# Kernel optimization log

Hardware: AMD Instinct MI355X
Metric: run time of the kernel (lower is better)

Reference implementation:

```python
import jax, jax.numpy as jnp
import numpy as np
from jax import lax

B, C, H, W = 4, 64, 96, 320
RC = C // 4                     # reduced channels = 16
D = 48                          # max_disp = len(norm_disp_range)
NORM_DISP = jnp.arange(D, dtype=jnp.float32) / 160.0
EPS = 1e-5


def conv2d(x, w, b=None, pad=0, groups=1):
    y = lax.conv_general_dilated(x, w, (1, 1), ((pad, pad), (pad, pad)),
                                 dimension_numbers=('NCHW', 'OIHW', 'NCHW'),
                                 feature_group_count=groups)
    if b is not None:
        y = y + b[None, :, None, None]
    return y


def group_norm(x, g, b, groups=8):
    n, c, h, w = x.shape
    xg = x.reshape(n, groups, c // groups, h, w)
    mu = xg.mean(axis=(2, 3, 4), keepdims=True)
    var = xg.var(axis=(2, 3, 4), keepdims=True)
    xn = ((xg - mu) * lax.rsqrt(var + EPS)).reshape(n, c, h, w)
    return xn * g[None, :, None, None] + b[None, :, None, None]


elu = jax.nn.elu


def setup_inputs() -> dict:
    key = jax.random.key(0)
    ks = iter(jax.random.split(key, 32))

    def rn(shape, scale=0.05):
        return jax.random.normal(next(ks), shape, dtype=jnp.float32) * scale

    inp = {
        'left_feat': jax.random.normal(next(ks), (B, C, H, W), jnp.float32),
        'right_feat': jax.random.normal(next(ks), (B, C, H, W), jnp.float32),
        'directs': jnp.ones((B,), jnp.float32),
        # q_conv / k_conv: 1x1 conv (no bias) + GroupNorm(8) params
        'qw': rn((RC, C, 1, 1)), 'q_g': jnp.ones((RC,)), 'q_b': jnp.zeros((RC,)),
        'kw': rn((RC, C, 1, 1)), 'k_g': jnp.ones((RC,)), 'k_b': jnp.zeros((RC,)),
        # global_attn: avgpool -> 1x1 (rc->rc/2) -> ELU -> 1x1 (rc/2->rc)
        'ga_w1': rn((RC // 2, RC, 1, 1)), 'ga_b1': jnp.zeros((RC // 2,)),
        'ga_w2': rn((RC, RC // 2, 1, 1)), 'ga_b2': jnp.zeros((RC,)),
        # local_attn: 3x3 conv + GN(8) + ELU
        'la_w': rn((RC, RC, 3, 3)), 'la_b': jnp.zeros((RC,)),
        'la_g': jnp.ones((RC,)), 'la_bb': jnp.zeros((RC,)),
        # attn_fusion: 1x1 (2rc->rc) -> ELU -> 1x1 (rc->D)
        'af_w1': rn((RC, 2 * RC, 1, 1)), 'af_b1': jnp.zeros((RC,)),
        'af_w2': rn((D, RC, 1, 1)), 'af_b2': jnp.zeros((D,)),
        # refine_cost: depthwise 3x3 (groups=D) -> ELU -> 1x1
        'rdw_w': rn((D, 1, 3, 3)), 'rdw_b': jnp.zeros((D,)),
        'rpw_w': rn((D, D, 1, 1)), 'rpw_b': jnp.zeros((D,)),
        # fusion: reflection-pad 3x3 conv (C+D -> C) + SELayer(C, 16)
        'fu_w': rn((C, C + D, 3, 3)), 'fu_b': jnp.zeros((C,)),
        'se_w1': rn((C // 16, C)), 'se_w2': rn((C, C // 16)),
    }
    return inp


def reference(left_feat, right_feat, directs, qw, q_g, q_b, kw, k_g, k_b,
              ga_w1, ga_b1, ga_w2, ga_b2, la_w, la_b, la_g, la_bb,
              af_w1, af_b1, af_w2, af_b2, rdw_w, rdw_b, rpw_w, rpw_b,
              fu_w, fu_b, se_w1, se_w2):
    q = elu(group_norm(conv2d(left_feat, qw), q_g, q_b))      # [B,RC,H,W]
    k = elu(group_norm(conv2d(right_feat, kw), k_g, k_b))     # [B,RC,H,W]

    gp = q.mean(axis=(2, 3), keepdims=True)                   # AdaptiveAvgPool2d(1)
    gfeat = conv2d(elu(conv2d(gp, ga_w1, ga_b1)), ga_w2, ga_b2)
    gfeat = jnp.broadcast_to(gfeat, q.shape)
    lfeat = elu(group_norm(conv2d(q, la_w, la_b, pad=1), la_g, la_bb))
    comb = jnp.concatenate([gfeat, lfeat], axis=1)            # [B,2RC,H,W]
    attn = conv2d(elu(conv2d(comb, af_w1, af_b1)), af_w2, af_b2)  # [B,D,H,W]

    # Warped cost volume. grid_sample shifts only the x-coordinate by
    # disp*2*directs (normalized, align_corners=True), i.e. a constant
    # horizontal shift of disp*directs*(W-1) pixels with border clamping.
    # Channel-mean commutes with horizontal bilinear sampling, so warp
    # the channel-mean map directly (identical math, D x less work).
    km = k.mean(axis=1)                                       # [B,H,W]
    shift = NORM_DISP[None, :] * directs[:, None] * (W - 1)   # [B,D]
    pos = jnp.arange(W, dtype=jnp.float32)[None, None, :] + shift[:, :, None]  # [B,D,W]
    x0 = jnp.floor(pos)
    f = pos - x0                                              # bilinear frac
    i0 = jnp.clip(x0, 0, W - 1).astype(jnp.int32)
    i1 = jnp.clip(x0 + 1, 0, W - 1).astype(jnp.int32)

    def gather(idx):  # km[b,h,idx[b,d,w]] -> [B,D,H,W]
        return jnp.take_along_axis(
            km[:, None, :, :],
            jnp.broadcast_to(idx[:, :, None, :], (B, D, H, W)), axis=3)

    fw = f[:, :, None, :]
    warped = gather(i0) * (1.0 - fw) + gather(i1) * fw        # [B,D,H,W]
    vol = warped * jax.nn.sigmoid(attn)                       # sigmoid-weighted volume

    cost = conv2d(elu(conv2d(vol, rdw_w, rdw_b, pad=1, groups=D)), rpw_w, rpw_b)
    norm_cost = jax.nn.softmax(cost, axis=1)

    # fusion: ReflectionPad2d(1) + 3x3 conv, SE layer, ELU
    cat = jnp.concatenate([left_feat, norm_cost], axis=1)     # [B,C+D,H,W]
    cat_p = jnp.pad(cat, ((0, 0), (0, 0), (1, 1), (1, 1)), mode='reflect')
    fused = conv2d(cat_p, fu_w, fu_b)                         # [B,C,H,W]
    y = fused.mean(axis=(2, 3))                               # [B,C]
    y = jax.nn.sigmoid(jax.nn.relu(y @ se_w1.T) @ se_w2.T)
    x = elu(fused * y[:, :, None, None])
    return (x, norm_cost)
```

## Files before the change

kernel.cpp:

```cpp
#include <hip/hip_runtime.h>
#include <math.h>

static constexpr int B_  = 4;
static constexpr int C_  = 64;
static constexpr int H_  = 96;
static constexpr int W_  = 320;
static constexpr int HW  = H_ * W_;
static constexpr int RCH = 16;
static constexpr int D_  = 48;
static constexpr int NG  = 8;
static constexpr int CPG = RCH / NG;
static constexpr float EPS_ = 1e-5f;
static constexpr int APX = 322;

typedef __attribute__((ext_vector_type(8))) short short8;
typedef __attribute__((ext_vector_type(4))) float f32x4;
typedef __attribute__((ext_vector_type(4))) unsigned int u32x4;

__device__ __forceinline__ float elu1(float x) { return x > 0.f ? x : __expf(x) - 1.f; }
__device__ __forceinline__ float sigm(float x) { return 1.f / (1.f + __expf(-x)); }
__device__ __forceinline__ unsigned bf16rne(float f) {
    unsigned u = __builtin_bit_cast(unsigned, f);
    u += 0x7fffu + ((u >> 16) & 1u);
    return u >> 16;
}
__device__ __forceinline__ void gload16(const void* g, void* l) {
    __builtin_amdgcn_global_load_lds((const __attribute__((address_space(1))) unsigned int*)g,
                                     (__attribute__((address_space(3))) unsigned int*)l, 16, 0, 0);
}

__global__ __launch_bounds__(256) void k_wrepack(
    const float* __restrict__ qw, const float* __restrict__ kw, const float* __restrict__ law,
    float* __restrict__ qwp, float* __restrict__ kwp, float* __restrict__ lawp)
{
    int t = threadIdx.x;
    for (int i = t; i < RCH * C_; i += 256) {
        int c = i >> 4, r = i & 15;
        qwp[i] = qw[r * C_ + c];
        kwp[i] = kw[r * C_ + c];
    }
    for (int i = t; i < RCH * RCH * 9; i += 256) {
        int co = i & 15, rest = i >> 4;
        int ci = rest / 9, tap = rest % 9;
        lawp[i] = law[(co * RCH + ci) * 9 + tap];
    }
}

__global__ __launch_bounds__(256) void k_conv_qk(
    const float* __restrict__ left, const float* __restrict__ right,
    const float* __restrict__ qwp, const float* __restrict__ kwp,
    float* __restrict__ qraw, float* __restrict__ kraw)
{
    int idx = blockIdx.x * 256 + threadIdx.x;
    int half = idx / (B_ * HW / 2);
    int r0 = idx - half * (B_ * HW / 2);
    int b = r0 / (HW / 2), p2 = r0 - b * (HW / 2);
    int p = p2 * 2;
    const float* src = (half ? right : left) + (size_t)b * C_ * HW + p;
    const float* wp  = half ? kwp : qwp;
    float* dst = (half ? kraw : qraw) + (size_t)b * RCH * HW + p;
    float2 acc[RCH];
#pragma unroll
    for (int r = 0; r < RCH; r++) acc[r] = make_float2(0.f, 0.f);
#pragma unroll
    for (int c = 0; c < C_; c++) {
        float2 v = *reinterpret_cast<const float2*>(src + (size_t)c * HW);
        const float* wrow = wp + c * RCH;
#pragma unroll
        for (int r = 0; r < RCH; r++) {
            acc[r].x += v.x * wrow[r];
            acc[r].y += v.y * wrow[r];
        }
    }
#pragma unroll
    for (int r = 0; r < RCH; r++)
        *reinterpret_cast<float2*>(dst + (size_t)r * HW) = acc[r];
}

__global__ __launch_bounds__(256) void k_gn_stats2(const float* __restrict__ qsrc,
    const float* __restrict__ ksrc, float* __restrict__ stats)
{
    int z = blockIdx.x;
    const float* src = (z < 32) ? qsrc : ksrc;
    int zz = (z < 32) ? z : z - 32;
    int b = zz / NG, g = zz % NG;
    const float4* base = (const float4*)(src + ((size_t)b * RCH + g * CPG) * HW);
    float s = 0.f, ss = 0.f;
    for (int i = threadIdx.x; i < CPG * HW / 4; i += 256) {
        float4 v = base[i];
        s  += v.x + v.y + v.z + v.w;
        ss += v.x * v.x + v.y * v.y + v.z * v.z + v.w * v.w;
    }
    __shared__ float rs[256], rq[256];
    rs[threadIdx.x] = s; rq[threadIdx.x] = ss; __syncthreads();
    for (int off = 128; off > 0; off >>= 1) {
        if (threadIdx.x < off) { rs[threadIdx.x] += rs[threadIdx.x + off]; rq[threadIdx.x] += rq[threadIdx.x + off]; }
        __syncthreads();
    }
    if (threadIdx.x == 0) {
        float inv = 1.f / (float)(CPG * HW);
        float m = rs[0] * inv;
        float var = rq[0] * inv - m * m;
        stats[z * 2 + 0] = m;
        stats[z * 2 + 1] = rsqrtf(var + EPS_);
    }
}

__global__ __launch_bounds__(256) void k_gn_stats(const float* __restrict__ src, float* __restrict__ stats)
{
    int b = blockIdx.x / NG, g = blockIdx.x % NG;
    const float4* base = (const float4*)(src + ((size_t)b * RCH + g * CPG) * HW);
    float s = 0.f, ss = 0.f;
    for (int i = threadIdx.x; i < CPG * HW / 4; i += 256) {
        float4 v = base[i];
        s  += v.x + v.y + v.z + v.w;
        ss += v.x * v.x + v.y * v.y + v.z * v.z + v.w * v.w;
    }
    __shared__ float rs[256], rq[256];
    rs[threadIdx.x] = s; rq[threadIdx.x] = ss; __syncthreads();
    for (int off = 128; off > 0; off >>= 1) {
        if (threadIdx.x < off) { rs[threadIdx.x] += rs[threadIdx.x + off]; rq[threadIdx.x] += rq[threadIdx.x + off]; }
        __syncthreads();
    }
    if (threadIdx.x == 0) {
        float inv = 1.f / (float)(CPG * HW);
        float m = rs[0] * inv;
        float var = rq[0] * inv - m * m;
        stats[blockIdx.x * 2 + 0] = m;
        stats[blockIdx.x * 2 + 1] = rsqrtf(var + EPS_);
    }
}

__global__ __launch_bounds__(256) void k_gn_apply(float* __restrict__ x, const float* __restrict__ stats,
    const float* __restrict__ gam, const float* __restrict__ bet)
{
    int idx4 = blockIdx.x * 256 + threadIdx.x;
    int b = idx4 / (RCH * HW / 4);
    int rc = (idx4 / (HW / 4)) % RCH;
    int g = rc >> 1;
    float m = stats[(b * NG + g) * 2], is = stats[(b * NG + g) * 2 + 1];
    float ga = gam[rc] * is, be = bet[rc] - m * is * gam[rc];
    float4 v = ((const float4*)x)[idx4];
    v.x = elu1(v.x * ga + be); v.y = elu1(v.y * ga + be);
    v.z = elu1(v.z * ga + be); v.w = elu1(v.w * ga + be);
    ((float4*)x)[idx4] = v;
}

__global__ __launch_bounds__(256) void k_km(const float* __restrict__ kraw, const float* __restrict__ stats,
    const float* __restrict__ gam, const float* __restrict__ bet, float* __restrict__ km)
{
    int idx = blockIdx.x * 256 + threadIdx.x;
    int b = idx / HW, p = idx - b * HW;
    float s = 0.f;
#pragma unroll
    for (int rc = 0; rc < RCH; rc++) {
        int g = rc >> 1;
        float m = stats[(b * NG + g) * 2], is = stats[(b * NG + g) * 2 + 1];
        float v = (kraw[((size_t)b * RCH + rc) * HW + p] - m) * is * gam[rc] + bet[rc];
        s += elu1(v);
    }
    km[idx] = s * (1.f / (float)RCH);
}

__global__ __launch_bounds__(256) void k_rowmean(const float* __restrict__ src, float* __restrict__ out)
{
    const float4* base = (const float4*)(src + (size_t)blockIdx.x * HW);
    float s = 0.f;
    for (int p = threadIdx.x; p < HW / 4; p += 256) {
        float4 v = base[p];
        s += v.x + v.y + v.z + v.w;
    }
    __shared__ float red[256];
    red[threadIdx.x] = s; __syncthreads();
    for (int off = 128; off > 0; off >>= 1) {
        if (threadIdx.x < off) red[threadIdx.x] += red[threadIdx.x + off];
        __syncthreads();
    }
    if (threadIdx.x == 0) out[blockIdx.x] = red[0] * (1.f / (float)HW);
}

__global__ __launch_bounds__(64) void k_gfeat(const float* __restrict__ gp,
    const float* __restrict__ gaw1, const float* __restrict__ gab1,
    const float* __restrict__ gaw2, const float* __restrict__ gab2,
    const float* __restrict__ afw1, const float* __restrict__ afb1,
    float* __restrict__ gbias)
{
    __shared__ float g1[B_ * 8], gf[B_ * RCH];
    int t = threadIdx.x;
    if (t < B_ * 8) {
        int b = t >> 3, o = t & 7;
        float a = gab1[o];
        for (int i = 0; i < RCH; i++) a += gaw1[o * RCH + i] * gp[b * RCH + i];
        g1[b * 8 + o] = elu1(a);
    }
    __syncthreads();
    {
        int b = t >> 4, o = t & 15;
        float a = gab2[o];
        for (int i = 0; i < 8; i++) a += gaw2[o * 8 + i] * g1[b * 8 + i];
        gf[t] = a;
    }
    __syncthreads();
    {
        int b = t >> 4, o = t & 15;
        float a = afb1[o];
        for (int i = 0; i < RCH; i++) a += afw1[o * 2 * RCH + i] * gf[b * RCH + i];
        gbias[t] = a;
    }
}

__global__ __launch_bounds__(256) void k_conv_la(const float* __restrict__ q,
    const float* __restrict__ lawp, const float* __restrict__ lab, float* __restrict__ lraw)
{
    int idx = blockIdx.x * 256 + threadIdx.x;
    int b = idx / HW, p = idx - b * HW;
    int h = p / W_, w = p - h * W_;
    float acc[RCH];
#pragma unroll
    for (int co = 0; co < RCH; co++) acc[co] = lab[co];
#pragma unroll
    for (int ci = 0; ci < RCH; ci++) {
        const float* qb = q + ((size_t)b * RCH + ci) * HW;
#pragma unroll
        for (int kh = 0; kh < 3; kh++) {
            int hh = h + kh - 1;
            if (hh < 0 || hh >= H_) continue;
            float a0 = (w - 1 >= 0) ? qb[hh * W_ + w - 1] : 0.f;
            float a1 = qb[hh * W_ + w];
            float a2 = (w + 1 < W_) ? qb[hh * W_ + w + 1] : 0.f;
            const float* wp0 = lawp + (ci * 9 + kh * 3) * RCH;
#pragma unroll
            for (int co = 0; co < RCH; co++)
                acc[co] += a0 * wp0[co] + a1 * wp0[RCH + co] + a2 * wp0[2 * RCH + co];
        }
    }
#pragma unroll
    for (int co = 0; co < RCH; co++) lraw[((size_t)b * RCH + co) * HW + p] = acc[co];
}

__global__ __launch_bounds__(320) void k_vol(const float* __restrict__ lraw,
    const float* __restrict__ stats, const float* __restrict__ lg, const float* __restrict__ lb,
    const float* __restrict__ gbias, const float* __restrict__ afw1,
    const float* __restrict__ afw2, const float* __restrict__ afb2,
    const float* __restrict__ km, const float* __restrict__ directs, float* __restrict__ vol)
{
    __shared__ float w1[RCH * 2 * RCH];
    __shared__ float w2[D_ * RCH];
    __shared__ float b2[D_];
    __shared__ float kms[W_];
    int blk = blockIdx.x;
    int b = blk / H_, h = blk - b * H_;
    int t = threadIdx.x;
    for (int i = t; i < RCH * 2 * RCH; i += 320) w1[i] = afw1[i];
    for (int i = t; i < D_ * RCH; i += 320) w2[i] = afw2[i];
    if (t < D_) b2[t] = afb2[t];
    kms[t] = km[(size_t)b * HW + h * W_ + t];
    __syncthreads();
    int w = t, p = h * W_ + w;
    float lf[RCH];
#pragma unroll
    for (int rc = 0; rc < RCH; rc++) {
        int g = rc >> 1;
        float m = stats[(b * NG + g) * 2], is = stats[(b * NG + g) * 2 + 1];
        lf[rc] = elu1((lraw[((size_t)b * RCH + rc) * HW + p] - m) * is * lg[rc] + lb[rc]);
    }
    float hid[RCH];
#pragma unroll
    for (int o = 0; o < RCH; o++) {
        float a = gbias[b * RCH + o];
#pragma unroll
        for (int i = 0; i < RCH; i++) a += w1[o * 2 * RCH + RCH + i] * lf[i];
        hid[o] = elu1(a);
    }
    float dir = directs[b];
    for (int d = 0; d < D_; d++) {
        float a = b2[d];
#pragma unroll
        for (int o = 0; o < RCH; o++) a += w2[d * RCH + o] * hid[o];
        float s = sigm(a);
        float shift = ((float)d / 160.f) * dir * (float)(W_ - 1);
        float pos = (float)w + shift;
        float x0 = floorf(pos);
        float f = pos - x0;
        float c0 = fminf(fmaxf(x0, 0.f), (float)(W_ - 1));
        float c1 = fminf(fmaxf(x0 + 1.f, 0.f), (float)(W_ - 1));
        int i0 = (int)c0, i1 = (int)c1;
        float wv = kms[i0] * (1.f - f) + kms[i1] * f;
        vol[((size_t)(b * D_ + d)) * HW + p] = wv * s;
    }
}

__global__ __launch_bounds__(256) void k_dw(const float* __restrict__ vol,
    const float* __restrict__ wgt, const float* __restrict__ bias, float* __restrict__ dwout)
{
    int idx = blockIdx.x * 256 + threadIdx.x;
    int p4 = idx % (HW / 4);
    int d  = (idx / (HW / 4)) % D_;
    int b  = idx / (D_ * HW / 4);
    int h = p4 / (W_ / 4), w = (p4 % (W_ / 4)) * 4;
    const float* vb = vol + ((size_t)(b * D_ + d)) * HW;
    float wz[9];
#pragma unroll
    for (int i = 0; i < 9; i++) wz[i] = wgt[d * 9 + i];
    float bv = bias[d];
    float acc[4] = {bv, bv, bv, bv};
#pragma unroll
    for (int r = 0; r < 3; r++) {
        int hh = h + r - 1;
        if (hh < 0 || hh >= H_) continue;
        const float* row = vb + hh * W_;
        float4 c = *(const float4*)(row + w);
        float in6[6];
        in6[0] = (w > 0) ? row[w - 1] : 0.f;
        in6[1] = c.x; in6[2] = c.y; in6[3] = c.z; in6[4] = c.w;
        in6[5] = (w + 4 < W_) ? row[w + 4] : 0.f;
#pragma unroll
        for (int j = 0; j < 4; j++)
            acc[j] += in6[j] * wz[r * 3] + in6[j + 1] * wz[r * 3 + 1] + in6[j + 2] * wz[r * 3 + 2];
    }
    float4 o;
    o.x = elu1(acc[0]); o.y = elu1(acc[1]); o.z = elu1(acc[2]); o.w = elu1(acc[3]);
    ((float4*)dwout)[idx] = o;
}

__global__ __launch_bounds__(256) void k_prep(const float* __restrict__ left, unsigned int* __restrict__ abf)
{
    int idx = blockIdx.x * 256 + threadIdx.x;
    int px = idx % APX;
    int bh = idx / APX;
    int b = bh / H_, h = bh % H_;
    int w = px - 1;
    w = w < 0 ? -w : (w >= W_ ? 2 * W_ - 2 - w : w);
    const float* src = left + (size_t)b * C_ * HW + h * W_ + w;
    unsigned int* dst = abf + (size_t)idx * 60;
#pragma unroll
    for (int q4 = 0; q4 < 8; q4++) {
        u32x4 t;
#pragma unroll
        for (int z = 0; z < 4; z++) {
            int ci = (q4 * 4 + z) * 2;
            float f0 = src[(size_t)ci * HW];
            float f1 = src[(size_t)(ci + 1) * HW];
            t[z] = bf16rne(f0) | (bf16rne(f1) << 16);
        }
        *reinterpret_cast<u32x4*>(dst + q4 * 4) = t;
    }
    *reinterpret_cast<u32x4*>(dst + 56) = (u32x4){0u, 0u, 0u, 0u};
}

__global__ __launch_bounds__(256) void k_rpw(float* __restrict__ ncost,
    const float* __restrict__ wgt, const float* __restrict__ bias,
    unsigned int* __restrict__ abf)
{
    __shared__ float wr[D_ * D_];
    __shared__ float bs[D_];
    for (int i = threadIdx.x; i < D_ * D_; i += 256) wr[i] = wgt[i];
    if (threadIdx.x < D_) bs[threadIdx.x] = bias[threadIdx.x];
    __syncthreads();
    int idx = blockIdx.x * 256 + threadIdx.x;
    int b = idx / HW, p = idx - b * HW;
    int h = p / W_, w = p - h * W_;
    float v[D_];
#pragma unroll
    for (int i = 0; i < D_; i++) v[i] = ncost[((size_t)(b * D_ + i)) * HW + p];
    float cst[D_];
    float mx = -1e30f;
#pragma unroll
    for (int d = 0; d < D_; d++) {
        float a = bs[d];
        const float4* wrow = (const float4*)&wr[d * D_];
#pragma unroll
        for (int i4 = 0; i4 < D_ / 4; i4++) {
            float4 wv = wrow[i4];
            a += wv.x * v[i4 * 4 + 0] + wv.y * v[i4 * 4 + 1]
               + wv.z * v[i4 * 4 + 2] + wv.w * v[i4 * 4 + 3];
        }
        cst[d] = a; mx = fmaxf(mx, a);
    }
    float s = 0.f;
#pragma unroll
    for (int d = 0; d < D_; d++) { float e = __expf(cst[d] - mx); cst[d] = e; s += e; }
    float inv = 1.f / s;
#pragma unroll
    for (int d = 0; d < D_; d++) {
        cst[d] *= inv;
        ncost[((size_t)(b * D_ + d)) * HW + p] = cst[d];
    }
    u32x4 pk[6];
#pragma unroll
    for (int q4 = 0; q4 < 6; q4++)
#pragma unroll
        for (int z = 0; z < 4; z++) {
            int d = (q4 * 4 + z) * 2;
            pk[q4][z] = bf16rne(cst[d]) | (bf16rne(cst[d + 1]) << 16);
        }
    size_t bh322 = (size_t)(b * H_ + h) * APX;
    unsigned int* dst = abf + (bh322 + (w + 1)) * 60 + 32;
#pragma unroll
    for (int q4 = 0; q4 < 6; q4++) *reinterpret_cast<u32x4*>(dst + q4 * 4) = pk[q4];
    if (w == 1 || w == W_ - 2) {
        unsigned int* dst2 = abf + (bh322 + (w == 1 ? 0 : APX - 1)) * 60 + 32;
#pragma unroll
        for (int q4 = 0; q4 < 6; q4++) *reinterpret_cast<u32x4*>(dst2 + q4 * 4) = pk[q4];
    }
}

__global__ __launch_bounds__(256) void k_wpack(const float* __restrict__ fw, unsigned short* __restrict__ wpack,
    float* __restrict__ ymean)
{
    int bi = blockIdx.x;
    int t = threadIdx.x;
    if (bi == 0 && t < B_ * C_) ymean[t] = 0.f;
    int tap = bi >> 2, kblk = bi & 3;
    int kh = tap / 3, kw2 = tap % 3;
    int ct = t >> 6, l = t & 63;
    int co = ct * 16 + (l & 15);
    int ci0 = kblk * 32 + ((l >> 4) & 3) * 8;
    unsigned short v[8];
#pragma unroll
    for (int j = 0; j < 8; j++) {
        int ci = ci0 + j;
        float f = (ci < 112) ? fw[((size_t)(co * 112 + ci)) * 9 + kh * 3 + kw2] : 0.f;
        v[j] = (unsigned short)bf16rne(f);
    }
    *reinterpret_cast<short8*>(wpack + ((size_t)bi * 256 + t) * 8) = *reinterpret_cast<short8*>(v);
}

static constexpr int TPX    = 80;
static constexpr int LPXC   = TPX + 2;
static constexpr int LROWB  = 240;
static constexpr int LPLANB = LPXC * LROWB;
static constexpr int NPT    = TPX / 16;
__global__ __launch_bounds__(256, 1) void k_fused_mfma(
    const unsigned int* __restrict__ abf,
    const unsigned short* __restrict__ wpack, const float* __restrict__ fb,
    float* __restrict__ fused, float* __restrict__ ymean)
{
    __shared__ __align__(16) unsigned int Atile4[4 * LPXC * 60 + 4];
    int flat = blockIdx.x + 4 * (blockIdx.y + 48 * blockIdx.z);
    int tau = (flat & 7) * 96 + (flat >> 3);
    int wx = tau & 3, hy = (tau >> 2) % 48, bb = tau / 192;
    int h0 = hy * 2;
    int w0 = wx * TPX;
    int tid = threadIdx.x;
    int wid = tid >> 6;
    int l   = tid & 63;

    {
        int hh = h0 - 1 + wid;
        hh = hh < 0 ? -hh : (hh >= H_ ? 2 * H_ - 2 - hh : hh);
        const char* gsrc = (const char*)(abf + ((size_t)(bb * H_ + hh) * APX + w0) * 60);
        char* lbase = (char*)Atile4 + wid * LPLANB;
#pragma unroll
        for (int i = 0; i < 19; i++)
            gload16(gsrc + (i * 64 + l) * 16, lbase + i * 1024);
        if (l < 14) gload16(gsrc + (1216 + l) * 16, lbase + 1216 * 16);
    }
    __syncthreads();

    int row = wid >> 1;
    int ch  = wid & 1;
    int li = l & 15, lg = l >> 4;

    const short8* __restrict__ wp8 = reinterpret_cast<const short8*>(wpack);

    f32x4 acc[NPT][2];
    float bv0 = fb[(ch * 2 + 0) * 16 + li];
    float bv1 = fb[(ch * 2 + 1) * 16 + li];
#pragma unroll
    for (int pt = 0; pt < NPT; pt++) {
        acc[pt][0] = (f32x4){bv0, bv0, bv0, bv0};
        acc[pt][1] = (f32x4){bv1, bv1, bv1, bv1};
    }

    const char* Abase = (const char*)Atile4;
    short8 bc0 = wp8[0 * 256 + (ch * 2 + 0) * 64 + l];
    short8 bc1 = wp8[0 * 256 + (ch * 2 + 1) * 64 + l];
#pragma unroll
    for (int step = 0; step < 36; step++) {
        int kh = step / 12, kw2 = (step / 4) % 3, kblk = step & 3;
        short8 bn0 = bc0, bn1 = bc1;
        if (step < 35) {
            bn0 = wp8[(step + 1) * 256 + (ch * 2 + 0) * 64 + l];
            bn1 = wp8[(step + 1) * 256 + (ch * 2 + 1) * 64 + l];
        }
        int rbase = (row + kh) * LPLANB + kblk * 64 + lg * 16 + (kw2 + li) * LROWB;
        short8 av[NPT];
#pragma unroll
        for (int pt = 0; pt < NPT; pt++)
            av[pt] = *reinterpret_cast<const short8*>(Abase + rbase + pt * (16 * LROWB));
#pragma unroll
        for (int pt = 0; pt < NPT; pt++) {
            acc[pt][0] = __builtin_amdgcn_mfma_f32_16x16x32_bf16(av[pt], bc0, acc[pt][0], 0, 0, 0);
            acc[pt][1] = __builtin_amdgcn_mfma_f32_16x16x32_bf16(av[pt], bc1, acc[pt][1], 0, 0, 0);
        }
        bc0 = bn0; bc1 = bn1;
    }

    int h = h0 + row;
#pragma unroll
    for (int j = 0; j < 2; j++) {
        int co = (ch * 2 + j) * 16 + li;
        float* ob = fused + ((size_t)(bb * C_ + co) * H_ + h) * W_ + w0 + lg * 4;
#pragma unroll
        for (int pt = 0; pt < NPT; pt++) {
            *reinterpret_cast<f32x4*>(ob + pt * 16) = acc[pt][j];
        }
    }
    float s0 = 0.f, s1 = 0.f;
#pragma unroll
    for (int pt = 0; pt < NPT; pt++)
#pragma unroll
        for (int rg = 0; rg < 4; rg++) { s0 += acc[pt][0][rg]; s1 += acc[pt][1][rg]; }
    s0 += __shfl_xor(s0, 16); s0 += __shfl_xor(s0, 32);
    s1 += __shfl_xor(s1, 16); s1 += __shfl_xor(s1, 32);
    if (lg == 0) {
        atomicAdd(&ymean[bb * C_ + (ch * 2 + 0) * 16 + li], s0);
        atomicAdd(&ymean[bb * C_ + (ch * 2 + 1) * 16 + li], s1);
    }
}

__global__ __launch_bounds__(256) void k_se(const float* __restrict__ ymean,
    const float* __restrict__ w1, const float* __restrict__ w2, float* __restrict__ scale)
{
    __shared__ float h4[B_ * 4];
    int t = threadIdx.x;
    const float invHW = 1.f / (float)HW;
    if (t < B_ * 4) {
        int b = t >> 2, o = t & 3;
        float a = 0.f;
        for (int c = 0; c < C_; c++) a += w1[o * C_ + c] * (ymean[b * C_ + c] * invHW);
        h4[b * 4 + o] = fmaxf(a, 0.f);
    }
    __syncthreads();
    {
        int b = t >> 6, c = t & 63;
        float a = 0.f;
        for (int o = 0; o < 4; o++) a += w2[c * 4 + o] * h4[b * 4 + o];
        scale[t] = sigm(a);
    }
}

__global__ __launch_bounds__(256) void k_final(const float* __restrict__ fused,
    const float* __restrict__ scale, float* __restrict__ out)
{
    int idx4 = blockIdx.x * 256 + threadIdx.x;
    int bc = idx4 / (HW / 4);
    float sc = scale[bc];
    float4 v = ((const float4*)fused)[idx4];
    v.x = elu1(v.x * sc); v.y = elu1(v.y * sc);
    v.z = elu1(v.z * sc); v.w = elu1(v.w * sc);
    ((float4*)out)[idx4] = v;
}

extern "C" void kernel_launch(void* const* d_in, const int* in_sizes, int n_in,
                              void* d_out, int out_size, void* d_ws, size_t ws_size,
                              hipStream_t stream)
{
    const float* left   = (const float*)d_in[0];
    const float* right  = (const float*)d_in[1];
    const float* directs= (const float*)d_in[2];
    const float* qw     = (const float*)d_in[3];
    const float* q_g    = (const float*)d_in[4];
    const float* q_b    = (const float*)d_in[5];
    const float* kw     = (const float*)d_in[6];
    const float* k_g    = (const float*)d_in[7];
    const float* k_b    = (const float*)d_in[8];
    const float* gaw1   = (const float*)d_in[9];
    const float* gab1   = (const float*)d_in[10];
    const float* gaw2   = (const float*)d_in[11];
    const float* gab2   = (const float*)d_in[12];
    const float* law    = (const float*)d_in[13];
    const float* lab    = (const float*)d_in[14];
    const float* lag    = (const float*)d_in[15];
    const float* labb   = (const float*)d_in[16];
    const float* afw1   = (const float*)d_in[17];
    const float* afb1   = (const float*)d_in[18];
    const float* afw2   = (const float*)d_in[19];
    const float* afb2   = (const float*)d_in[20];
    const float* rdww   = (const float*)d_in[21];
    const float* rdwb   = (const float*)d_in[22];
    const float* rpww   = (const float*)d_in[23];
    const float* rpwb   = (const float*)d_in[24];
    const float* fuw    = (const float*)d_in[25];
    const float* fub    = (const float*)d_in[26];
    const float* sew1   = (const float*)d_in[27];
    const float* sew2   = (const float*)d_in[28];

    float* ws    = (float*)d_ws;
    float* qraw  = ws + 0;
    float* kraw  = ws + 1966080;
    float* km    = ws + 3932160;
    float* vol   = ws + 9953280;
    float* smal  = ws + 15851520;
    unsigned int* abf = (unsigned int*)(ws + 0);
    float* fused = ws + 7418880;
    float* lraw  = kraw;
    unsigned short* wpack = (unsigned short*)(ws + 15811584);

    float* qwp   = ws + 4055040;
    float* kwp   = ws + 4056064;
    float* lawp  = ws + 4057088;

    float* stQ   = smal + 0;
    float* stL   = smal + 128;
    float* gp    = smal + 192;
    float* gbias = smal + 256;
    float* ymean = smal + 320;
    float* scal  = smal + 576;

    float* xout  = (float*)d_out;
    float* ncost = xout + 7864320;

    k_wrepack<<<1, 256, 0, stream>>>(qw, kw, law, qwp, kwp, lawp);
    k_conv_qk<<<480, 256, 0, stream>>>(left, right, qwp, kwp, qraw, kraw);
    k_gn_stats2<<<64, 256, 0, stream>>>(qraw, kraw, stQ);
    k_gn_apply<<<1920, 256, 0, stream>>>(qraw, stQ, q_g, q_b);
    k_km<<<480, 256, 0, stream>>>(kraw, stQ + 64, k_g, k_b, km);
    k_rowmean<<<64, 256, 0, stream>>>(qraw, gp);
    k_gfeat<<<1, 64, 0, stream>>>(gp, gaw1, gab1, gaw2, gab2, afw1, afb1, gbias);
    k_conv_la<<<480, 256, 0, stream>>>(qraw, lawp, lab, lraw);
    k_gn_stats<<<32, 256, 0, stream>>>(lraw, stL);
    k_vol<<<384, 320, 0, stream>>>(lraw, stL, lag, labb, gbias, afw1, afw2, afb2, km, directs, vol);
    k_dw<<<5760, 256, 0, stream>>>(vol, rdww, rdwb, ncost);
    k_prep<<<483, 256, 0, stream>>>(left, abf);
    k_rpw<<<480, 256, 0, stream>>>(ncost, rpww, rpwb, abf);
    k_wpack<<<36, 256, 0, stream>>>(fuw, wpack, ymean);
    k_fused_mfma<<<dim3(4, 48, 4), 256, 0, stream>>>(abf, wpack, fub, fused, ymean);
    k_se<<<1, 256, 0, stream>>>(ymean, sew1, sew2, scal);
    k_final<<<7680, 256, 0, stream>>>(fused, scal, xout);
}
```

Before: 248.9 us.

## Fuse bf16 left-feature packing into q/k conv, merge weight prep, store fused as bf16

The bf16 packing of left features for the fusion conv now happens inside the q/k 1x1 conv kernel, which already reads those values, so the separate k_prep kernel and its second read of left_feat are gone. The weight repack and the fusion-weight pack kernels are merged into one launch. The fusion conv output is stored as bf16 instead of fp32, which halves the intermediate traffic through k_final but adds rounding error to the final output. The workspace layout is reshuffled so the new buffers do not overlap live data.

```diff
diff --git a/kernel.cpp b/kernel.cpp
--- a/kernel.cpp
+++ b/kernel.cpp
@@ -16,6 +16,7 @@
 typedef __attribute__((ext_vector_type(8))) short short8;
 typedef __attribute__((ext_vector_type(4))) float f32x4;
 typedef __attribute__((ext_vector_type(4))) unsigned int u32x4;
+typedef __attribute__((ext_vector_type(4))) unsigned short u16x4;
 
 __device__ __forceinline__ float elu1(float x) { return x > 0.f ? x : __expf(x) - 1.f; }
 __device__ __forceinline__ float sigm(float x) { return 1.f / (1.f + __expf(-x)); }
@@ -24,53 +25,104 @@
     u += 0x7fffu + ((u >> 16) & 1u);
     return u >> 16;
 }
+__device__ __forceinline__ float bf2f(unsigned short u) {
+    unsigned v = ((unsigned)u) << 16;
+    return __builtin_bit_cast(float, v);
+}
 __device__ __forceinline__ void gload16(const void* g, void* l) {
     __builtin_amdgcn_global_load_lds((const __attribute__((address_space(1))) unsigned int*)g,
                                      (__attribute__((address_space(3))) unsigned int*)l, 16, 0, 0);
 }
 
-__global__ __launch_bounds__(256) void k_wrepack(
+__global__ __launch_bounds__(256) void k_wprep(
     const float* __restrict__ qw, const float* __restrict__ kw, const float* __restrict__ law,
-    float* __restrict__ qwp, float* __restrict__ kwp, float* __restrict__ lawp)
-{
+    const float* __restrict__ fw,
+    float* __restrict__ qwp, float* __restrict__ kwp, float* __restrict__ lawp,
+    unsigned short* __restrict__ wpack, float* __restrict__ ymean)
+{
+    int bi = blockIdx.x;
     int t = threadIdx.x;
-    for (int i = t; i < RCH * C_; i += 256) {
-        int c = i >> 4, r = i & 15;
-        qwp[i] = qw[r * C_ + c];
-        kwp[i] = kw[r * C_ + c];
-    }
-    for (int i = t; i < RCH * RCH * 9; i += 256) {
-        int co = i & 15, rest = i >> 4;
-        int ci = rest / 9, tap = rest % 9;
-        lawp[i] = law[(co * RCH + ci) * 9 + tap];
-    }
+    if (bi == 36) {
+        if (t < B_ * C_) ymean[t] = 0.f;
+        for (int i = t; i < RCH * C_; i += 256) {
+            int c = i >> 4, r = i & 15;
+            qwp[i] = qw[r * C_ + c];
+            kwp[i] = kw[r * C_ + c];
+        }
+        for (int i = t; i < RCH * RCH * 9; i += 256) {
+            int co = i & 15, rest = i >> 4;
+            int ci = rest / 9, tap = rest % 9;
+            lawp[i] = law[(co * RCH + ci) * 9 + tap];
+        }
+        return;
+    }
+    int tap = bi >> 2, kblk = bi & 3;
+    int kh = tap / 3, kw2 = tap % 3;
+    int ct = t >> 6, l = t & 63;
+    int co = ct * 16 + (l & 15);
+    int ci0 = kblk * 32 + ((l >> 4) & 3) * 8;
+    unsigned short v[8];
+#pragma unroll
+    for (int j = 0; j < 8; j++) {
+        int ci = ci0 + j;
+        float f = (ci < 112) ? fw[((size_t)(co * 112 + ci)) * 9 + kh * 3 + kw2] : 0.f;
+        v[j] = (unsigned short)bf16rne(f);
+    }
+    *reinterpret_cast<short8*>(wpack + ((size_t)bi * 256 + t) * 8) = *reinterpret_cast<short8*>(v);
 }
 
 __global__ __launch_bounds__(256) void k_conv_qk(
     const float* __restrict__ left, const float* __restrict__ right,
     const float* __restrict__ qwp, const float* __restrict__ kwp,
-    float* __restrict__ qraw, float* __restrict__ kraw)
+    float* __restrict__ qraw, float* __restrict__ kraw, unsigned int* __restrict__ abf)
 {
     int idx = blockIdx.x * 256 + threadIdx.x;
     int half = idx / (B_ * HW / 2);
     int r0 = idx - half * (B_ * HW / 2);
     int b = r0 / (HW / 2), p2 = r0 - b * (HW / 2);
     int p = p2 * 2;
+    int h = p / W_, w = p - h * W_;
     const float* src = (half ? right : left) + (size_t)b * C_ * HW + p;
     const float* wp  = half ? kwp : qwp;
     float* dst = (half ? kraw : qraw) + (size_t)b * RCH * HW + p;
+    size_t bh322 = (size_t)(b * H_ + h) * APX;
+    unsigned int* dstA = abf + (bh322 + (w + 1)) * 60;
     float2 acc[RCH];
 #pragma unroll
     for (int r = 0; r < RCH; r++) acc[r] = make_float2(0.f, 0.f);
 #pragma unroll
-    for (int c = 0; c < C_; c++) {
-        float2 v = *reinterpret_cast<const float2*>(src + (size_t)c * HW);
-        const float* wrow = wp + c * RCH;
-#pragma unroll
-        for (int r = 0; r < RCH; r++) {
-            acc[r].x += v.x * wrow[r];
-            acc[r].y += v.y * wrow[r];
-        }
+    for (int cg = 0; cg < 8; cg++) {
+        float2 v[8];
+#pragma unroll
+        for (int j = 0; j < 8; j++) v[j] = *reinterpret_cast<const float2*>(src + (size_t)(cg * 8 + j) * HW);
+#pragma unroll
+        for (int j = 0; j < 8; j++) {
+            const float* wrow = wp + (cg * 8 + j) * RCH;
+#pragma unroll
+            for (int r = 0; r < RCH; r++) {
+                acc[r].x += v[j].x * wrow[r];
+                acc[r].y += v[j].y * wrow[r];
+            }
+        }
+        if (half == 0) {
+            u32x4 t0, t1;
+#pragma unroll
+            for (int z = 0; z < 4; z++) {
+                t0[z] = bf16rne(v[2 * z].x) | (bf16rne(v[2 * z + 1].x) << 16);
+                t1[z] = bf16rne(v[2 * z].y) | (bf16rne(v[2 * z + 1].y) << 16);
+            }
+            *reinterpret_cast<u32x4*>(dstA + cg * 4) = t0;
+            *reinterpret_cast<u32x4*>(dstA + 60 + cg * 4) = t1;
+            if (w == 0)      *reinterpret_cast<u32x4*>(abf + bh322 * 60 + cg * 4) = t1;
+            if (w == W_ - 2) *reinterpret_cast<u32x4*>(abf + (bh322 + APX - 1) * 60 + cg * 4) = t0;
+        }
+    }
+    if (half == 0) {
+        u32x4 zz = (u32x4){0u, 0u, 0u, 0u};
+        *reinterpret_cast<u32x4*>(dstA + 56) = zz;
+        *reinterpret_cast<u32x4*>(dstA + 116) = zz;
+        if (w == 0)      *reinterpret_cast<u32x4*>(abf + bh322 * 60 + 56) = zz;
+        if (w == W_ - 2) *reinterpret_cast<u32x4*>(abf + (bh322 + APX - 1) * 60 + 56) = zz;
     }
 #pragma unroll
     for (int r = 0; r < RCH; r++)
@@ -323,31 +375,6 @@
     ((float4*)dwout)[idx] = o;
 }
 
-__global__ __launch_bounds__(256) void k_prep(const float* __restrict__ left, unsigned int* __restrict__ abf)
-{
-    int idx = blockIdx.x * 256 + threadIdx.x;
-    int px = idx % APX;
-    int bh = idx / APX;
-    int b = bh / H_, h = bh % H_;
-    int w = px - 1;
-    w = w < 0 ? -w : (w >= W_ ? 2 * W_ - 2 - w : w);
-    const float* src = left + (size_t)b * C_ * HW + h * W_ + w;
-    unsigned int* dst = abf + (size_t)idx * 60;
-#pragma unroll
-    for (int q4 = 0; q4 < 8; q4++) {
-        u32x4 t;
-#pragma unroll
-        for (int z = 0; z < 4; z++) {
-            int ci = (q4 * 4 + z) * 2;
-            float f0 = src[(size_t)ci * HW];
-            float f1 = src[(size_t)(ci + 1) * HW];
-            t[z] = bf16rne(f0) | (bf16rne(f1) << 16);
-        }
-        *reinterpret_cast<u32x4*>(dst + q4 * 4) = t;
-    }
-    *reinterpret_cast<u32x4*>(dst + 56) = (u32x4){0u, 0u, 0u, 0u};
-}
-
 __global__ __launch_bounds__(256) void k_rpw(float* __restrict__ ncost,
     const float* __restrict__ wgt, const float* __restrict__ bias,
     unsigned int* __restrict__ abf)
@@ -405,27 +432,6 @@
     }
 }
 
-__global__ __launch_bounds__(256) void k_wpack(const float* __restrict__ fw, unsigned short* __restrict__ wpack,
-    float* __restrict__ ymean)
-{
-    int bi = blockIdx.x;
-    int t = threadIdx.x;
-    if (bi == 0 && t < B_ * C_) ymean[t] = 0.f;
-    int tap = bi >> 2, kblk = bi & 3;
-    int kh = tap / 3, kw2 = tap % 3;
-    int ct = t >> 6, l = t & 63;
-    int co = ct * 16 + (l & 15);
-    int ci0 = kblk * 32 + ((l >> 4) & 3) * 8;
-    unsigned short v[8];
-#pragma unroll
-    for (int j = 0; j < 8; j++) {
-        int ci = ci0 + j;
-        float f = (ci < 112) ? fw[((size_t)(co * 112 + ci)) * 9 + kh * 3 + kw2] : 0.f;
-        v[j] = (unsigned short)bf16rne(f);
-    }
-    *reinterpret_cast<short8*>(wpack + ((size_t)bi * 256 + t) * 8) = *reinterpret_cast<short8*>(v);
-}
-
 static constexpr int TPX    = 80;
 static constexpr int LPXC   = TPX + 2;
 static constexpr int LROWB  = 240;
@@ -434,7 +440,7 @@
 __global__ __launch_bounds__(256, 1) void k_fused_mfma(
     const unsigned int* __restrict__ abf,
     const unsigned short* __restrict__ wpack, const float* __restrict__ fb,
-    float* __restrict__ fused, float* __restrict__ ymean)
+    unsigned short* __restrict__ fusedB, float* __restrict__ ymean)
 {
     __shared__ __align__(16) unsigned int Atile4[4 * LPXC * 60 + 4];
     int flat = blockIdx.x + 4 * (blockIdx.y + 48 * blockIdx.z);
@@ -501,10 +507,13 @@
 #pragma unroll
     for (int j = 0; j < 2; j++) {
         int co = (ch * 2 + j) * 16 + li;
-        float* ob = fused + ((size_t)(bb * C_ + co) * H_ + h) * W_ + w0 + lg * 4;
+        unsigned short* ob = fusedB + ((size_t)(bb * C_ + co) * H_ + h) * W_ + w0 + lg * 4;
 #pragma unroll
         for (int pt = 0; pt < NPT; pt++) {
-            *reinterpret_cast<f32x4*>(ob + pt * 16) = acc[pt][j];
+            u16x4 pk;
+#pragma unroll
+            for (int rg = 0; rg < 4; rg++) pk[rg] = (unsigned short)bf16rne(acc[pt][j][rg]);
+            *reinterpret_cast<u16x4*>(ob + pt * 16) = pk;
         }
     }
     float s0 = 0.f, s1 = 0.f;
@@ -541,16 +550,24 @@
     }
 }
 
-__global__ __launch_bounds__(256) void k_final(const float* __restrict__ fused,
+__global__ __launch_bounds__(256) void k_final(const unsigned short* __restrict__ fusedB,
     const float* __restrict__ scale, float* __restrict__ out)
 {
-    int idx4 = blockIdx.x * 256 + threadIdx.x;
-    int bc = idx4 / (HW / 4);
+    int idx8 = blockIdx.x * 256 + threadIdx.x;
+    int bc = idx8 / (HW / 8);
     float sc = scale[bc];
-    float4 v = ((const float4*)fused)[idx4];
-    v.x = elu1(v.x * sc); v.y = elu1(v.y * sc);
-    v.z = elu1(v.z * sc); v.w = elu1(v.w * sc);
-    ((float4*)out)[idx4] = v;
+    short8 v = ((const short8*)fusedB)[idx8];
+    float4 o0, o1;
+    o0.x = elu1(bf2f((unsigned short)v[0]) * sc);
+    o0.y = elu1(bf2f((unsigned short)v[1]) * sc);
+    o0.z = elu1(bf2f((unsigned short)v[2]) * sc);
+    o0.w = elu1(bf2f((unsigned short)v[3]) * sc);
+    o1.x = elu1(bf2f((unsigned short)v[4]) * sc);
+    o1.y = elu1(bf2f((unsigned short)v[5]) * sc);
+    o1.z = elu1(bf2f((unsigned short)v[6]) * sc);
+    o1.w = elu1(bf2f((unsigned short)v[7]) * sc);
+    ((float4*)out)[idx8 * 2 + 0] = o0;
+    ((float4*)out)[idx8 * 2 + 1] = o1;
 }
 
 extern "C" void kernel_launch(void* const* d_in, const int* in_sizes, int n_in,
@@ -588,19 +605,18 @@
     const float* sew2   = (const float*)d_in[28];
 
     float* ws    = (float*)d_ws;
-    float* qraw  = ws + 0;
-    float* kraw  = ws + 1966080;
-    float* km    = ws + 3932160;
-    float* vol   = ws + 9953280;
+    unsigned int* abf = (unsigned int*)(ws + 0);
+    float* kraw  = ws + 7418880;
+    float* lraw  = kraw;
+    float* km    = ws + 9384960;
+    float* qraw  = ws + 9507840;
+    float* vol   = ws + 9507840;
+    unsigned short* fusedB = (unsigned short*)(ws + 7418880);
+    float* qwp   = ws + 15406080;
+    float* kwp   = ws + 15407104;
+    float* lawp  = ws + 15408128;
+    unsigned short* wpack = (unsigned short*)(ws + 15410432);
     float* smal  = ws + 15851520;
-    unsigned int* abf = (unsigned int*)(ws + 0);
-    float* fused = ws + 7418880;
-    float* lraw  = kraw;
-    unsigned short* wpack = (unsigned short*)(ws + 15811584);
-
-    float* qwp   = ws + 4055040;
-    float* kwp   = ws + 4056064;
-    float* lawp  = ws + 4057088;
 
     float* stQ   = smal + 0;
     float* stL   = smal + 128;
@@ -612,8 +628,8 @@
     float* xout  = (float*)d_out;
     float* ncost = xout + 7864320;
 
-    k_wrepack<<<1, 256, 0, stream>>>(qw, kw, law, qwp, kwp, lawp);
-    k_conv_qk<<<480, 256, 0, stream>>>(left, right, qwp, kwp, qraw, kraw);
+    k_wprep<<<37, 256, 0, stream>>>(qw, kw, law, fuw, qwp, kwp, lawp, wpack, ymean);
+    k_conv_qk<<<480, 256, 0, stream>>>(left, right, qwp, kwp, qraw, kraw, abf);
     k_gn_stats2<<<64, 256, 0, stream>>>(qraw, kraw, stQ);
     k_gn_apply<<<1920, 256, 0, stream>>>(qraw, stQ, q_g, q_b);
     k_km<<<480, 256, 0, stream>>>(kraw, stQ + 64, k_g, k_b, km);
@@ -623,10 +639,8 @@
     k_gn_stats<<<32, 256, 0, stream>>>(lraw, stL);
     k_vol<<<384, 320, 0, stream>>>(lraw, stL, lag, labb, gbias, afw1, afw2, afb2, km, directs, vol);
     k_dw<<<5760, 256, 0, stream>>>(vol, rdww, rdwb, ncost);
-    k_prep<<<483, 256, 0, stream>>>(left, abf);
     k_rpw<<<480, 256, 0, stream>>>(ncost, rpww, rpwb, abf);
-    k_wpack<<<36, 256, 0, stream>>>(fuw, wpack, ymean);
-    k_fused_mfma<<<dim3(4, 48, 4), 256, 0, stream>>>(abf, wpack, fub, fused, ymean);
+    k_fused_mfma<<<dim3(4, 48, 4), 256, 0, stream>>>(abf, wpack, fub, fusedB, ymean);
     k_se<<<1, 256, 0, stream>>>(ymean, sew1, sew2, scal);
-    k_final<<<7680, 256, 0, stream>>>(fused, scal, xout);
-}
+    k_final<<<3840, 256, 0, stream>>>(fusedB, scal, xout);
+}
```

Result: slower. 433.7 us (+74.2%).
